# Performance work log

Measured on AMD Instinct MI355X. Metric: run time of the kernel, lower is better.

The kernel has to match this reference:

```python
import jax, jax.numpy as jnp
import numpy as np
from jax import lax

NB = 8          # num_blocks
THRESH = 0.01   # sparsity_threshold


def _clinear(z, wr, wi, bias):
    # complex linear y = z @ W^T + b with W = wr + i*wi, z complex
    # (c+id)(a+ib) = (ca - db) + i(cb + da)  -- same math as the torch
    # Karatsuba decomposition (k1-k3, k1+k2).
    zr, zi = z.real, z.imag
    yr = jnp.einsum('...i,oi->...o', zr, wr) - jnp.einsum('...i,oi->...o', zi, wi)
    yi = jnp.einsum('...i,oi->...o', zr, wi) + jnp.einsum('...i,oi->...o', zi, wr)
    y = lax.complex(yr, yi)
    return y + lax.complex(bias[:, 0], bias[:, 1])


def _softshrink(v, t):
    return jnp.where(v > t, v - t, jnp.where(v < -t, v + t, jnp.zeros_like(v)))


def setup_inputs() -> dict:
    key = jax.random.key(0)
    ks = jax.random.split(key, 7)
    B, H, W, D = 4, 128, 128, 768
    bs = D // NB          # block_size = 96
    hid = bs              # hidden_size_factor = 1.0
    scale = np.sqrt(0.5).astype(np.float32)
    kaiming = 1.0 / np.sqrt(bs)
    x = jax.random.normal(ks[0], (B, H, W, D), dtype=jnp.float32)
    # ComplexLinear weights: nn.Linear init then scaled by sqrt(0.5)
    w1r = jax.random.uniform(ks[1], (hid, bs), jnp.float32, -kaiming, kaiming) * scale
    w1i = jax.random.uniform(ks[2], (hid, bs), jnp.float32, -kaiming, kaiming) * scale
    b1 = jax.random.normal(ks[3], (hid, 2), dtype=jnp.float32) * 0.02
    kaiming2 = 1.0 / np.sqrt(hid)
    w2r = jax.random.uniform(ks[4], (bs, hid), jnp.float32, -kaiming2, kaiming2) * scale
    w2i = jax.random.uniform(ks[5], (bs, hid), jnp.float32, -kaiming2, kaiming2) * scale
    b2 = jax.random.normal(ks[6], (bs, 2), dtype=jnp.float32) * 0.02
    return {"x": x, "w1r": w1r, "w1i": w1i, "b1": b1,
            "w2r": w2r, "w2i": w2i, "b2": b2}


def reference(x, w1r, w1i, b1, w2r, w2i, b2):
    B, H, W, D = x.shape
    bs = D // NB
    bias = x  # direct_skip=True -> identity skip
    # ortho-normalized real FFT over spatial dims (1,2)
    xf = jnp.fft.rfftn(x, s=(H, W), axes=(1, 2), norm='ortho')  # [B,H,Fw,D] c64
    Fw = xf.shape[2]
    xb = xf.reshape(B, H, Fw, NB, bs)
    h = _clinear(xb, w1r, w1i, b1)
    h = lax.complex(jax.nn.relu(h.real), jax.nn.relu(h.imag))  # ComplexReLU
    y = _clinear(h, w2r, w2i, b2)
    y = y.reshape(B, H, Fw, D)
    # componentwise softshrink (by_magnitude=False)
    y = lax.complex(_softshrink(y.real, THRESH), _softshrink(y.imag, THRESH))
    out = jnp.fft.irfftn(y, s=(H, W), axes=(1, 2), norm='ortho')
    return out + bias
```

## Files before the change

### kernel.cpp

```cpp
#include <hip/hip_runtime.h>
#include <hip/hip_bf16.h>
#include <cstdio>

#define TPB 256
#define B_ 4
#define H_ 128
#define W_ 128
#define D_ 768
#define FW 65
#define BH_ 512
#define THRESH_ 0.01f
#define NEG_TWO_PI_OVER_128 (-0.04908738521234052f)

typedef short bf16x8 __attribute__((ext_vector_type(8)));
typedef float f32x4 __attribute__((ext_vector_type(4)));
typedef float f32x2 __attribute__((ext_vector_type(2)));


__device__ __forceinline__ unsigned pk(float lo, float hi) {
  __hip_bfloat162 h2 = __float22bfloat162_rn(make_float2(lo, hi));
  return *(unsigned*)&h2;
}
__device__ __forceinline__ float2 upk(unsigned u) {
  return __bfloat1622float2(*(__hip_bfloat162*)&u);
}
__device__ __forceinline__ int drev(int k) {
  return ((k & 3) << 5) | (((k >> 2) & 3) << 3) | (((k >> 4) & 3) << 1) | ((k >> 6) & 1);
}
__device__ __forceinline__ int drevinv(int s) {
  return ((s & 1) << 6) | (((s >> 1) & 3) << 4) | (((s >> 3) & 3) << 2) | ((s >> 5) & 3);
}

template <bool FWD>
__device__ __forceinline__ void bf4reg(float& x0r, float& x0i, float& x1r, float& x1i,
                                       float& x2r, float& x2i, float& x3r, float& x3i,
                                       float c1, float s1, float c2, float s2, float c3, float s3) {
  const float v0r = x0r + x2r, v0i = x0i + x2i, v2r = x0r - x2r, v2i = x0i - x2i;
  const float v1r = x1r + x3r, v1i = x1i + x3i, v3r = x1r - x3r, v3i = x1i - x3i;
  float u1r, u1i, u3r, u3i;
  if (FWD) { u1r = v2r + v3i; u1i = v2i - v3r; u3r = v2r - v3i; u3i = v2i + v3r; }
  else     { u1r = v2r - v3i; u1i = v2i + v3r; u3r = v2r + v3i; u3i = v2i - v3r; }
  const float u2r = v0r - v1r, u2i = v0i - v1i;
  x0r = v0r + v1r;            x0i = v0i + v1i;
  x1r = u1r * c1 - u1i * s1;  x1i = u1r * s1 + u1i * c1;
  x2r = u2r * c2 - u2i * s2;  x2i = u2r * s2 + u2i * c2;
  x3r = u3r * c3 - u3i * s3;  x3i = u3r * s3 + u3i * c3;
}

__device__ __forceinline__ void ibf4r(float& x0r, float& x0i, float& x1r, float& x1i,
                                      float& x2r, float& x2i, float& x3r, float& x3i,
                                      float c1, float s1, float c2, float s2, float c3, float s3) {
  const float t0r = x0r, t0i = x0i;
  const float t1r = x1r * c1 + x1i * s1, t1i = x1i * c1 - x1r * s1;
  const float t2r = x2r * c2 + x2i * s2, t2i = x2i * c2 - x2r * s2;
  const float t3r = x3r * c3 + x3i * s3, t3i = x3i * c3 - x3r * s3;
  const float w0r = t0r + t2r, w0i = t0i + t2i, w2r = t0r - t2r, w2i = t0i - t2i;
  const float w1r = t1r + t3r, w1i = t1i + t3i, w3r = t1r - t3r, w3i = t1i - t3i;
  x0r = w0r + w1r; x0i = w0i + w1i;
  x1r = w2r - w3i; x1i = w2i + w3r;
  x2r = w0r - w1r; x2i = w0i - w1i;
  x3r = w2r + w3i; x3i = w2i - w3r;
}

#define TW_INIT() do { if (t < 128) { float s_, c_; \
    __sincosf(NEG_TWO_PI_OVER_128 * (float)t, &s_, &c_); twr[t] = c_; twi[t] = s_; } } while (0)

__global__ __launch_bounds__(TPB) void k_wpack(const float* __restrict__ w1r,
                                               const float* __restrict__ w1i,
                                               const float* __restrict__ w2r,
                                               const float* __restrict__ w2i,
                                               unsigned short* __restrict__ wp) {
  const int tid = blockIdx.x * TPB + threadIdx.x;
  if (tid >= 2 * 36864) return;
  const int L = tid / 36864, rem = tid % 36864;
  const int n = rem / 192, k = rem % 192;
  const int c = k >> 1, s = k & 1, o = n >> 1, t = n & 1;
  const float* wr = L ? w2r : w1r;
  const float* wi = L ? w2i : w1i;
  const float val = (s == 0) ? (t == 0 ? wr[o * 96 + c] : wi[o * 96 + c])
                             : (t == 0 ? -wi[o * 96 + c] : wr[o * 96 + c]);
  __hip_bfloat16 h = __float2bfloat16(val);
  const int idx = ((n * 6 + (k >> 5)) * 4 + ((k >> 3) & 3)) * 8 + (k & 7);
  wp[L * 36864 + idx] = *(unsigned short*)&h;
}

__global__ __launch_bounds__(TPB) void k_fwd_w(const float* __restrict__ x,
                                               unsigned* __restrict__ fq) {
  __shared__ float re[4096], im[4096], twr[128], twi[128];
  const int t = threadIdx.x;
  const int bh = blockIdx.x;
  const int d0 = blockIdx.y << 6;
  TW_INIT();
  const int c = t & 31, p = t >> 5;
  const f32x2* xp = (const f32x2*)(x + (size_t)bh * 98304 + d0);

  float vr[4][4], vi[4][4];
#pragma unroll
  for (int q = 0; q < 4; ++q)
#pragma unroll
    for (int m = 0; m < 4; ++m) {
      const f32x2 v = __builtin_nontemporal_load(&xp[(p + 8 * m + 32 * q) * 384 + c]);
      vr[q][m] = v.x; vi[q][m] = v.y;
    }
  __syncthreads();
#pragma unroll
  for (int m = 0; m < 4; ++m) {
    const int np = p + 8 * m;
    bf4reg<true>(vr[0][m], vi[0][m], vr[1][m], vi[1][m], vr[2][m], vi[2][m], vr[3][m], vi[3][m],
                 twr[np], twi[np], twr[2 * np], twi[2 * np], twr[3 * np], twi[3 * np]);
  }
#pragma unroll
  for (int q = 0; q < 4; ++q)
    bf4reg<true>(vr[q][0], vi[q][0], vr[q][1], vi[q][1], vr[q][2], vi[q][2], vr[q][3], vi[q][3],
                 twr[4 * p], twi[4 * p], twr[8 * p], twi[8 * p], twr[12 * p], twi[12 * p]);
#pragma unroll
  for (int q = 0; q < 4; ++q)
#pragma unroll
    for (int m = 0; m < 4; ++m) {
      const int pos = p + 8 * m + 32 * q;
      re[pos * 32 + c] = vr[q][m]; im[pos * 32 + c] = vi[q][m];
    }
  __syncthreads();

#pragma unroll
  for (int half = 0; half < 2; ++half) {
    const int g = 8 * half + p;
    float wr8[8], wi8[8];
#pragma unroll
    for (int j = 0; j < 8; ++j) { wr8[j] = re[(8 * g + j) * 32 + c]; wi8[j] = im[(8 * g + j) * 32 + c]; }
    bf4reg<true>(wr8[0], wi8[0], wr8[2], wi8[2], wr8[4], wi8[4], wr8[6], wi8[6],
                 1.f, 0.f, 1.f, 0.f, 1.f, 0.f);
    bf4reg<true>(wr8[1], wi8[1], wr8[3], wi8[3], wr8[5], wi8[5], wr8[7], wi8[7],
                 twr[16], twi[16], twr[32], twi[32], twr[48], twi[48]);
#pragma unroll
    for (int j = 0; j < 8; j += 2) {
      const float ar = wr8[j], ai = wi8[j], br = wr8[j + 1], bi = wi8[j + 1];
      wr8[j] = ar + br; wi8[j] = ai + bi;
      wr8[j + 1] = ar - br; wi8[j + 1] = ai - bi;
    }
#pragma unroll
    for (int j = 0; j < 8; ++j) {
      re[(8 * g + j) * 32 + c] = wr8[j]; im[(8 * g + j) * 32 + c] = wi8[j];
    }
  }
  __syncthreads();

#pragma unroll
  for (int it = 0; it < 9; ++it) {
    const int idx = it * TPB + t;
    if (idx < FW * 32) {
      const int q = idx >> 5, cc = idx & 31;
      const int sq = drev(q), smm = drev((128 - q) & 127);
      const float a = re[sq * 32 + cc], b = im[sq * 32 + cc];
      const float cr = re[smm * 32 + cc], dr = -im[smm * 32 + cc];
      const float hsc = 0.00390625f;
      const float xer = (a + cr) * hsc, xei = (b + dr) * hsc;
      const float xor_ = (b - dr) * hsc, xoi = (cr - a) * hsc;
      *(uint2*)(fq + (size_t)(bh * FW + q) * 768 + d0 + 2 * cc) =
          make_uint2(pk(xer, xei), pk(xor_, xoi));
    }
  }
}

__global__ __launch_bounds__(TPB) void k_fwd_h(unsigned* __restrict__ fq) {
  __shared__ float re[4096], im[4096], twr[128], twi[128];
  const int t = threadIdx.x;
  const int b = blockIdx.x, fw = blockIdx.y, d0 = blockIdx.z << 5;
  TW_INIT();
  unsigned* fp = fq + (size_t)(b * 128 * FW + fw) * 768 + d0;
  const int c = t & 31, p = t >> 5;
  const size_t hs = (size_t)FW * 768;

  float vr[4][4], vi[4][4];
#pragma unroll
  for (int q = 0; q < 4; ++q)
#pragma unroll
    for (int m = 0; m < 4; ++m) {
      const float2 v = upk(fp[(size_t)(p + 8 * m + 32 * q) * hs + c]);
      vr[q][m] = v.x; vi[q][m] = v.y;
    }
  __syncthreads();
#pragma unroll
  for (int m = 0; m < 4; ++m) {
    const int np = p + 8 * m;
    bf4reg<true>(vr[0][m], vi[0][m], vr[1][m], vi[1][m], vr[2][m], vi[2][m], vr[3][m], vi[3][m],
                 twr[np], twi[np], twr[2 * np], twi[2 * np], twr[3 * np], twi[3 * np]);
  }
#pragma unroll
  for (int q = 0; q < 4; ++q)
    bf4reg<true>(vr[q][0], vi[q][0], vr[q][1], vi[q][1], vr[q][2], vi[q][2], vr[q][3], vi[q][3],
                 twr[4 * p], twi[4 * p], twr[8 * p], twi[8 * p], twr[12 * p], twi[12 * p]);
#pragma unroll
  for (int q = 0; q < 4; ++q)
#pragma unroll
    for (int m = 0; m < 4; ++m) {
      const int pos = p + 8 * m + 32 * q;
      re[pos * 32 + c] = vr[q][m]; im[pos * 32 + c] = vi[q][m];
    }
  __syncthreads();

#pragma unroll
  for (int half = 0; half < 2; ++half) {
    const int g = 8 * half + p;
    float wr8[8], wi8[8];
#pragma unroll
    for (int j = 0; j < 8; ++j) { wr8[j] = re[(8 * g + j) * 32 + c]; wi8[j] = im[(8 * g + j) * 32 + c]; }
    bf4reg<true>(wr8[0], wi8[0], wr8[2], wi8[2], wr8[4], wi8[4], wr8[6], wi8[6],
                 1.f, 0.f, 1.f, 0.f, 1.f, 0.f);
    bf4reg<true>(wr8[1], wi8[1], wr8[3], wi8[3], wr8[5], wi8[5], wr8[7], wi8[7],
                 twr[16], twi[16], twr[32], twi[32], twr[48], twi[48]);
#pragma unroll
    for (int j = 0; j < 8; j += 2) {
      const float ar = wr8[j], ai = wi8[j], br = wr8[j + 1], bi = wi8[j + 1];
      wr8[j] = ar + br; wi8[j] = ai + bi;
      wr8[j + 1] = ar - br; wi8[j + 1] = ai - bi;
    }
#pragma unroll
    for (int j = 0; j < 8; ++j)
      fp[(size_t)(8 * g + j) * hs + c] = pk(wr8[j], wi8[j]);
  }
}

__global__ __launch_bounds__(TPB, 4) void k_mlp_mfma(unsigned* __restrict__ fq,
    const bf16x8* __restrict__ wpb,
    const float* __restrict__ b1, const float* __restrict__ b2) {
  __shared__ __align__(16) char lds[24576];
  const int t  = threadIdx.x;
  const int wv = t >> 6;
  const int l  = t & 63;
  const int c16 = l & 15, g = l >> 4, low3 = l & 7;
  const int n0 = wv * 48;
  const int P0 = blockIdx.x << 6;

  const uint4* src = (const uint4*)(fq + (size_t)P0 * 96);
#pragma unroll
  for (int it = 0; it < 6; ++it) {
    const int q = it * TPB + t;
    const int row = q / 24, f = q % 24;
    *(uint4*)(lds + row * 384 + ((f * 16) ^ ((row & 7) << 4))) = src[q];
  }
  __syncthreads();

  f32x4 acc[4][3];
  float bs0 = b1[n0 + c16], bs1 = b1[n0 + 16 + c16], bs2 = b1[n0 + 32 + c16];

#pragma unroll
  for (int mt = 0; mt < 4; ++mt)
#pragma unroll
    for (int np = 0; np < 3; ++np) acc[mt][np] = (f32x4)0.f;
  for (int kk = 0; kk < 6; ++kk) {
    bf16x8 a[4];
#pragma unroll
    for (int mt = 0; mt < 4; ++mt) {
      const int row = (mt << 4) + c16;
      a[mt] = *(const bf16x8*)(lds + row * 384 + ((kk * 64 + g * 16) ^ (low3 << 4)));
    }
    bf16x8 bfr[3];
#pragma unroll
    for (int np = 0; np < 3; ++np) bfr[np] = wpb[((n0 + np * 16 + c16) * 6 + kk) * 4 + g];
#pragma unroll
    for (int mt = 0; mt < 4; ++mt)
#pragma unroll
      for (int np = 0; np < 3; ++np)
        acc[mt][np] = __builtin_amdgcn_mfma_f32_16x16x32_bf16(a[mt], bfr[np], acc[mt][np], 0, 0, 0);
  }
  __syncthreads();
#pragma unroll
  for (int mt = 0; mt < 4; ++mt)
#pragma unroll
    for (int np = 0; np < 3; ++np) {
      const int col = n0 + np * 16 + c16;
      const float bb = np == 0 ? bs0 : (np == 1 ? bs1 : bs2);
#pragma unroll
      for (int r = 0; r < 4; ++r) {
        const int row = (mt << 4) + (g << 2) + r;
        const float vv = fmaxf(acc[mt][np][r] + bb, 0.f);
        __hip_bfloat16 hb = __float2bfloat16(vv);
        *(unsigned short*)(lds + row * 384 + ((2 * col) ^ ((row & 7) << 4))) = *(unsigned short*)&hb;
      }
    }
  __syncthreads();

  bs0 = b2[n0 + c16]; bs1 = b2[n0 + 16 + c16]; bs2 = b2[n0 + 32 + c16];
#pragma unroll
  for (int mt = 0; mt < 4; ++mt)
#pragma unroll
    for (int np = 0; np < 3; ++np) acc[mt][np] = (f32x4)0.f;
  const bf16x8* wpb2 = wpb + 4608;
  for (int kk = 0; kk < 6; ++kk) {
    bf16x8 a[4];
#pragma unroll
    for (int mt = 0; mt < 4; ++mt) {
      const int row = (mt << 4) + c16;
      a[mt] = *(const bf16x8*)(lds + row * 384 + ((kk * 64 + g * 16) ^ (low3 << 4)));
    }
    bf16x8 bfr[3];
#pragma unroll
    for (int np = 0; np < 3; ++np) bfr[np] = wpb2[((n0 + np * 16 + c16) * 6 + kk) * 4 + g];
#pragma unroll
    for (int mt = 0; mt < 4; ++mt)
#pragma unroll
      for (int np = 0; np < 3; ++np)
        acc[mt][np] = __builtin_amdgcn_mfma_f32_16x16x32_bf16(a[mt], bfr[np], acc[mt][np], 0, 0, 0);
  }
  unsigned short* fq16 = (unsigned short*)fq;
#pragma unroll
  for (int mt = 0; mt < 4; ++mt)
#pragma unroll
    for (int np = 0; np < 3; ++np) {
      const int col = n0 + np * 16 + c16;
      const float bb = np == 0 ? bs0 : (np == 1 ? bs1 : bs2);
#pragma unroll
      for (int r = 0; r < 4; ++r) {
        const int row = (mt << 4) + (g << 2) + r;
        float vv = acc[mt][np][r] + bb;
        vv = (vv > THRESH_) ? (vv - THRESH_) : ((vv < -THRESH_) ? (vv + THRESH_) : 0.f);
        __hip_bfloat16 hb = __float2bfloat16(vv);
        fq16[(size_t)(P0 + row) * 192 + col] = *(unsigned short*)&hb;
      }
    }
}

__global__ __launch_bounds__(TPB) void k_inv_h(unsigned* __restrict__ fq) {
  __shared__ float re[4096], im[4096], twr[128], twi[128];
  const int t = threadIdx.x;
  const int b = blockIdx.x, fw = blockIdx.y, d0 = blockIdx.z << 5;
  TW_INIT();
  unsigned* fp = fq + (size_t)(b * 128 * FW + fw) * 768 + d0;
  const int c = t & 31, p = t >> 5;
  const size_t hs = (size_t)FW * 768;

#pragma unroll
  for (int half = 0; half < 2; ++half) {
    const int g = 8 * half + p;
    float wr8[8], wi8[8];
#pragma unroll
    for (int j = 0; j < 8; ++j) {
      const float2 v = upk(fp[(size_t)(8 * g + j) * hs + c]);
      wr8[j] = v.x; wi8[j] = v.y;
    }
    if (half == 0) __syncthreads();
#pragma unroll
    for (int j = 0; j < 8; j += 2) {
      const float ar = wr8[j], ai = wi8[j], br = wr8[j + 1], bi = wi8[j + 1];
      wr8[j] = ar + br; wi8[j] = ai + bi;
      wr8[j + 1] = ar - br; wi8[j + 1] = ai - bi;
    }
    ibf4r(wr8[0], wi8[0], wr8[2], wi8[2], wr8[4], wi8[4], wr8[6], wi8[6],
          1.f, 0.f, 1.f, 0.f, 1.f, 0.f);
    ibf4r(wr8[1], wi8[1], wr8[3], wi8[3], wr8[5], wi8[5], wr8[7], wi8[7],
          twr[16], twi[16], twr[32], twi[32], twr[48], twi[48]);
#pragma unroll
    for (int j = 0; j < 8; ++j) {
      re[(8 * g + j) * 32 + c] = wr8[j]; im[(8 * g + j) * 32 + c] = wi8[j];
    }
  }
  __syncthreads();

  float vr[4][4], vi[4][4];
#pragma unroll
  for (int q = 0; q < 4; ++q)
#pragma unroll
    for (int m = 0; m < 4; ++m) {
      const int pos = p + 8 * m + 32 * q;
      vr[q][m] = re[pos * 32 + c]; vi[q][m] = im[pos * 32 + c];
    }
#pragma unroll
  for (int q = 0; q < 4; ++q)
    ibf4r(vr[q][0], vi[q][0], vr[q][1], vi[q][1], vr[q][2], vi[q][2], vr[q][3], vi[q][3],
          twr[4 * p], twi[4 * p], twr[8 * p], twi[8 * p], twr[12 * p], twi[12 * p]);
#pragma unroll
  for (int m = 0; m < 4; ++m) {
    const int np = p + 8 * m;
    ibf4r(vr[0][m], vi[0][m], vr[1][m], vi[1][m], vr[2][m], vi[2][m], vr[3][m], vi[3][m],
          twr[np], twi[np], twr[2 * np], twi[2 * np], twr[3 * np], twi[3 * np]);
  }
#pragma unroll
  for (int q = 0; q < 4; ++q)
#pragma unroll
    for (int m = 0; m < 4; ++m)
      fp[(size_t)(p + 8 * m + 32 * q) * hs + c] = pk(vr[q][m], vi[q][m]);
}

__global__ __launch_bounds__(TPB) void k_inv_w(const unsigned* __restrict__ fq,
                                               const float* __restrict__ x,
                                               float* __restrict__ out) {
  __shared__ float re[4096], im[4096], twr[128], twi[128];
  const int t = threadIdx.x;
  const int bh = blockIdx.x;
  const int d0 = blockIdx.y << 6;
  TW_INIT();
  const int c = t & 31, p = t >> 5;
  const float sc = 0.0078125f;

#pragma unroll
  for (int it = 0; it < 9; ++it) {
    const int idx = it * TPB + t;
    if (idx < FW * 32) {
      const int q = idx >> 5, cc = idx & 31;
      const uint2 vv = *(const uint2*)(fq + (size_t)(bh * FW + q) * 768 + d0 + 2 * cc);
      const float2 e = upk(vv.x), o = upk(vv.y);
      re[q * 32 + cc] = (e.x - o.y) * sc; im[q * 32 + cc] = (e.y + o.x) * sc;
      if (q >= 1 && q <= 63) {
        re[(128 - q) * 32 + cc] = (e.x + o.y) * sc;
        im[(128 - q) * 32 + cc] = (o.x - e.y) * sc;
      }
    }
  }
  __syncthreads();

  float vr[4][4], vi[4][4];
#pragma unroll
  for (int q = 0; q < 4; ++q)
#pragma unroll
    for (int m = 0; m < 4; ++m) {
      const int pos = p + 8 * m + 32 * q;
      vr[q][m] = re[pos * 32 + c]; vi[q][m] = im[pos * 32 + c];
    }
#pragma unroll
  for (int m = 0; m < 4; ++m) {
    const int np = p + 8 * m;
    bf4reg<false>(vr[0][m], vi[0][m], vr[1][m], vi[1][m], vr[2][m], vi[2][m], vr[3][m], vi[3][m],
                  twr[np], -twi[np], twr[2 * np], -twi[2 * np], twr[3 * np], -twi[3 * np]);
  }
#pragma unroll
  for (int q = 0; q < 4; ++q)
    bf4reg<false>(vr[q][0], vi[q][0], vr[q][1], vi[q][1], vr[q][2], vi[q][2], vr[q][3], vi[q][3],
                  twr[4 * p], -twi[4 * p], twr[8 * p], -twi[8 * p], twr[12 * p], -twi[12 * p]);
#pragma unroll
  for (int q = 0; q < 4; ++q)
#pragma unroll
    for (int m = 0; m < 4; ++m) {
      const int pos = p + 8 * m + 32 * q;
      re[pos * 32 + c] = vr[q][m]; im[pos * 32 + c] = vi[q][m];
    }
  __syncthreads();

  const f32x2* xv = (const f32x2*)x;
  f32x2* ov = (f32x2*)out;
#pragma unroll
  for (int half = 0; half < 2; ++half) {
    const int g = 8 * half + p;
    float wr8[8], wi8[8];
#pragma unroll
    for (int j = 0; j < 8; ++j) { wr8[j] = re[(8 * g + j) * 32 + c]; wi8[j] = im[(8 * g + j) * 32 + c]; }
    bf4reg<false>(wr8[0], wi8[0], wr8[2], wi8[2], wr8[4], wi8[4], wr8[6], wi8[6],
                  1.f, 0.f, 1.f, 0.f, 1.f, 0.f);
    bf4reg<false>(wr8[1], wi8[1], wr8[3], wi8[3], wr8[5], wi8[5], wr8[7], wi8[7],
                  twr[16], -twi[16], twr[32], -twi[32], twr[48], -twi[48]);
#pragma unroll
    for (int j = 0; j < 8; j += 2) {
      const float ar = wr8[j], ai = wi8[j], br = wr8[j + 1], bi = wi8[j + 1];
      wr8[j] = ar + br; wi8[j] = ai + bi;
      wr8[j + 1] = ar - br; wi8[j + 1] = ai - bi;
    }
#pragma unroll
    for (int j = 0; j < 8; ++j) {
      const int w = drevinv(8 * g + j);
      const size_t fi = (size_t)bh * 49152 + w * 384 + (d0 >> 1) + c;
      const f32x2 s = __builtin_nontemporal_load(&xv[fi]);
      f32x2 o; o.x = wr8[j] + s.x; o.y = wi8[j] + s.y;
      __builtin_nontemporal_store(o, &ov[fi]);
    }
  }
}

extern "C" void kernel_launch(void* const* d_in, const int* in_sizes, int n_in,
                              void* d_out, int out_size, void* d_ws, size_t ws_size,
                              hipStream_t stream) {
  const float* x   = (const float*)d_in[0];
  const float* w1r = (const float*)d_in[1];
  const float* w1i = (const float*)d_in[2];
  const float* b1  = (const float*)d_in[3];
  const float* w2r = (const float*)d_in[4];
  const float* w2i = (const float*)d_in[5];
  const float* b2  = (const float*)d_in[6];
  unsigned* fq = (unsigned*)d_ws;
  float* out = (float*)d_out;

  const size_t need = (size_t)BH_ * FW * 768 * 4;
  if (ws_size < need) {
    fprintf(stderr, "kernel_launch: ws too small (%zu < %zu)\n", ws_size, need);
    return;
  }

  unsigned short* wp = (unsigned short*)d_out;

  k_wpack<<<dim3(288), TPB, 0, stream>>>(w1r, w1i, w2r, w2i, wp);
  k_fwd_w<<<dim3(BH_, 12), TPB, 0, stream>>>(x, fq);
  k_fwd_h<<<dim3(B_, FW, 24), TPB, 0, stream>>>(fq);
  k_mlp_mfma<<<dim3(4160), TPB, 0, stream>>>(fq, (const bf16x8*)wp, b1, b2);
  k_inv_h<<<dim3(B_, FW, 24), TPB, 0, stream>>>(fq);
  k_inv_w<<<dim3(BH_, 12), TPB, 0, stream>>>(fq, x, out);
}
```

Baseline: 309.9 us.

## Fold identity skip into spectral domain before inverse W-FFT

The forward W-axis FFT result is written a second time into a new workspace buffer. The inverse W kernel adds that stored spectrum to the processed one before its inverse transform, so by linearity the transform reproduces x plus the MLP output. This removes the fp32 read of x in the last kernel but adds a bf16 half-spectrum write and read of similar size. The skip path is now rounded to bf16, which adds error against the reference.

New measurement: 296.0 us. 4.5% less time.

```diff
diff --git a/kernel.cpp b/kernel.cpp
--- a/kernel.cpp
+++ b/kernel.cpp
@@ -85,7 +85,8 @@
 }
 
 __global__ __launch_bounds__(TPB) void k_fwd_w(const float* __restrict__ x,
-                                               unsigned* __restrict__ fq) {
+                                               unsigned* __restrict__ fq,
+                                               unsigned* __restrict__ fq2) {
   __shared__ float re[4096], im[4096], twr[128], twi[128];
   const int t = threadIdx.x;
   const int bh = blockIdx.x;
@@ -156,8 +157,10 @@
       const float hsc = 0.00390625f;
       const float xer = (a + cr) * hsc, xei = (b + dr) * hsc;
       const float xor_ = (b - dr) * hsc, xoi = (cr - a) * hsc;
-      *(uint2*)(fq + (size_t)(bh * FW + q) * 768 + d0 + 2 * cc) =
-          make_uint2(pk(xer, xei), pk(xor_, xoi));
+      const uint2 u = make_uint2(pk(xer, xei), pk(xor_, xoi));
+      const size_t off = (size_t)(bh * FW + q) * 768 + d0 + 2 * cc;
+      *(uint2*)(fq + off) = u;
+      *(uint2*)(fq2 + off) = u;
     }
   }
 }
@@ -383,7 +386,7 @@
 }
 
 __global__ __launch_bounds__(TPB) void k_inv_w(const unsigned* __restrict__ fq,
-                                               const float* __restrict__ x,
+                                               const unsigned* __restrict__ fq2,
                                                float* __restrict__ out) {
   __shared__ float re[4096], im[4096], twr[128], twi[128];
   const int t = threadIdx.x;
@@ -398,12 +401,17 @@
     const int idx = it * TPB + t;
     if (idx < FW * 32) {
       const int q = idx >> 5, cc = idx & 31;
-      const uint2 vv = *(const uint2*)(fq + (size_t)(bh * FW + q) * 768 + d0 + 2 * cc);
+      const size_t off = (size_t)(bh * FW + q) * 768 + d0 + 2 * cc;
+      const uint2 vv = *(const uint2*)(fq + off);
+      const uint2 xx = *(const uint2*)(fq2 + off);
       const float2 e = upk(vv.x), o = upk(vv.y);
-      re[q * 32 + cc] = (e.x - o.y) * sc; im[q * 32 + cc] = (e.y + o.x) * sc;
+      const float2 e2 = upk(xx.x), o2 = upk(xx.y);
+      const float zer = e.x * sc + e2.x, zei = e.y * sc + e2.y;
+      const float zor = o.x * sc + o2.x, zoi = o.y * sc + o2.y;
+      re[q * 32 + cc] = zer - zoi; im[q * 32 + cc] = zei + zor;
       if (q >= 1 && q <= 63) {
-        re[(128 - q) * 32 + cc] = (e.x + o.y) * sc;
-        im[(128 - q) * 32 + cc] = (o.x - e.y) * sc;
+        re[(128 - q) * 32 + cc] = zer + zoi;
+        im[(128 - q) * 32 + cc] = zor - zei;
       }
     }
   }
@@ -436,7 +444,6 @@
     }
   __syncthreads();
 
-  const f32x2* xv = (const f32x2*)x;
   f32x2* ov = (f32x2*)out;
 #pragma unroll
   for (int half = 0; half < 2; ++half) {
@@ -458,8 +465,7 @@
     for (int j = 0; j < 8; ++j) {
       const int w = drevinv(8 * g + j);
       const size_t fi = (size_t)bh * 49152 + w * 384 + (d0 >> 1) + c;
-      const f32x2 s = __builtin_nontemporal_load(&xv[fi]);
-      f32x2 o; o.x = wr8[j] + s.x; o.y = wi8[j] + s.y;
+      f32x2 o; o.x = wr8[j]; o.y = wi8[j];
       __builtin_nontemporal_store(o, &ov[fi]);
     }
   }
@@ -475,10 +481,11 @@
   const float* w2r = (const float*)d_in[4];
   const float* w2i = (const float*)d_in[5];
   const float* b2  = (const float*)d_in[6];
-  unsigned* fq = (unsigned*)d_ws;
+  unsigned* fq  = (unsigned*)d_ws;
+  unsigned* fq2 = fq + (size_t)BH_ * FW * 768;
   float* out = (float*)d_out;
 
-  const size_t need = (size_t)BH_ * FW * 768 * 4;
+  const size_t need = (size_t)BH_ * FW * 768 * 4 * 2;
   if (ws_size < need) {
     fprintf(stderr, "kernel_launch: ws too small (%zu < %zu)\n", ws_size, need);
     return;
@@ -487,9 +494,9 @@
   unsigned short* wp = (unsigned short*)d_out;
 
   k_wpack<<<dim3(288), TPB, 0, stream>>>(w1r, w1i, w2r, w2i, wp);
-  k_fwd_w<<<dim3(BH_, 12), TPB, 0, stream>>>(x, fq);
+  k_fwd_w<<<dim3(BH_, 12), TPB, 0, stream>>>(x, fq, fq2);
   k_fwd_h<<<dim3(B_, FW, 24), TPB, 0, stream>>>(fq);
   k_mlp_mfma<<<dim3(4160), TPB, 0, stream>>>(fq, (const bf16x8*)wp, b1, b2);
   k_inv_h<<<dim3(B_, FW, 24), TPB, 0, stream>>>(fq);
-  k_inv_w<<<dim3(BH_, 12), TPB, 0, stream>>>(fq, x, out);
-}
+  k_inv_w<<<dim3(BH_, 12), TPB, 0, stream>>>(fq, fq2, out);
+}
```
